# Optimization experiments

Measured on AMD Instinct MI355X. Metric: run time of the kernel, lower is better.

The kernel has to match this reference:

```python
import jax, jax.numpy as jnp
import numpy as np

NEG_SLOPE = 0.2  # PyG GATv2Conv default negative_slope


def gatv2_layer(x, src, dst, Wl, bl, Wr, br, att, bias, concat):
    """GATv2Conv (PyG semantics): message j->i, softmax over incoming edges of i."""
    N = x.shape[0]
    H, C = att.shape
    xl = (x @ Wl + bl).reshape(N, H, C)  # source-side transform
    xr = (x @ Wr + br).reshape(N, H, C)  # target-side transform
    msg = xl[src]                                   # [E,H,C] gathered source feats
    e = jax.nn.leaky_relu(msg + xr[dst], NEG_SLOPE)  # [E,H,C]
    score = jnp.einsum('ehc,hc->eh', e, att)        # [E,H]
    # segment softmax over destination node (every node has a self loop -> no empty segment)
    smax = jax.ops.segment_max(score, dst, num_segments=N)
    ex = jnp.exp(score - smax[dst])
    denom = jax.ops.segment_sum(ex, dst, num_segments=N)
    alpha = ex / denom[dst]                         # [E,H]
    out = jax.ops.segment_sum(alpha[:, :, None] * msg, dst, num_segments=N)  # [N,H,C]
    out = out.reshape(N, H * C) if concat else out.mean(axis=1)
    return out + bias


def setup_inputs():
    key = jax.random.key(0)
    ks = jax.random.split(key, 16)
    N, E = 50000, 800000
    D_in, Hd, H, D_out = 128, 32, 4, 64
    HC = Hd * H  # 128
    s = 0.05
    return {
        'x': jax.random.normal(ks[0], (N, D_in), jnp.float32),
        'edge_index': jax.random.randint(ks[1], (2, E), 0, N, dtype=jnp.int32),
        # layer 1: GATv2Conv(D_in, Hd, heads=H)
        'Wl1': jax.random.normal(ks[2], (D_in, HC), jnp.float32) * s,
        'bl1': jnp.zeros((HC,), jnp.float32),
        'Wr1': jax.random.normal(ks[3], (D_in, HC), jnp.float32) * s,
        'br1': jnp.zeros((HC,), jnp.float32),
        'att1': jax.random.normal(ks[4], (H, Hd), jnp.float32) * s,
        'bias1': jnp.zeros((HC,), jnp.float32),
        # layer 2: GATv2Conv(HC, D_out, heads=1, concat=False)
        'Wl2': jax.random.normal(ks[5], (HC, D_out), jnp.float32) * s,
        'bl2': jnp.zeros((D_out,), jnp.float32),
        'Wr2': jax.random.normal(ks[6], (HC, D_out), jnp.float32) * s,
        'br2': jnp.zeros((D_out,), jnp.float32),
        'att2': jax.random.normal(ks[7], (1, D_out), jnp.float32) * s,
        'bias2': jnp.zeros((D_out,), jnp.float32),
    }


def reference(x, edge_index, Wl1, bl1, Wr1, br1, att1, bias1,
              Wl2, bl2, Wr2, br2, att2, bias2):
    N = x.shape[0]
    loops = jnp.arange(N, dtype=edge_index.dtype)  # add_self_loops=True (PyG default)
    src = jnp.concatenate([edge_index[0], loops])
    dst = jnp.concatenate([edge_index[1], loops])
    h = gatv2_layer(x, src, dst, Wl1, bl1, Wr1, br1, att1, bias1, concat=True)
    h = jax.nn.relu(h)
    out = gatv2_layer(h, src, dst, Wl2, bl2, Wr2, br2, att2, bias2, concat=False)
    return out
```

## Files before the change

kernel.cpp:

```cpp
#include <hip/hip_runtime.h>
#include <hip/hip_bf16.h>
#include <math.h>


#define NSLOPE 0.2f
#define L2E 1.4426950408889634f
#define BKT 64

typedef __attribute__((ext_vector_type(8))) short short8;
typedef __attribute__((ext_vector_type(4))) float f32x4;
typedef _Float16 h16x2 __attribute__((ext_vector_type(2)));

__device__ inline unsigned short f2bf(float f) {
  unsigned int u = __float_as_uint(f);
  u += 0x7fff + ((u >> 16) & 1);
  return (unsigned short)(u >> 16);
}
__device__ inline float bf2f(unsigned short h) {
  return __uint_as_float(((unsigned int)h) << 16);
}

__device__ inline float merge2(float qa, float qb, int m, int lane) {
  bool hi = (lane & m) != 0;
  float sel = hi ? qb : qa;
  float oth = hi ? qa : qb;
  return sel + __shfl_xor(oth, m);
}

template <typename AT>
__device__ __forceinline__ void gemm_body(const AT* __restrict__ A,
    const float* __restrict__ Wl, const float* __restrict__ Wr,
    const float* __restrict__ bl, const float* __restrict__ br,
    _Float16* __restrict__ xl, _Float16* __restrict__ xr, int C, int M,
    int mblk, int g, unsigned short* sBh, unsigned short* sBl) {
  int t = threadIdx.x;
  for (int s = t; s < 1024; s += 256) {
    int lane = s & 63;
    int kt = (s >> 6) & 3;
    int tn = s >> 8;
    int n = g * 64 + tn * 16 + (lane & 15);
    int k0 = kt * 32 + ((lane >> 4) * 8);
    const float* W = (n < C) ? (Wl + n) : (Wr + (n - C));
    int base = ((tn * 4 + kt) * 64 + lane) * 8;
#pragma unroll
    for (int j = 0; j < 8; j++) {
      float v = W[(size_t)(k0 + j) * C];
      unsigned short hi = f2bf(v);
      sBh[base + j] = hi;
      sBl[base + j] = f2bf(v - bf2f(hi));
    }
  }
  __syncthreads();
  int w = t >> 6, l = t & 63;
  int m_base = mblk * 128 + w * 32;
  int mrow = l & 15;
  int kq = l >> 4;
  f32x4 acc[2][4];
#pragma unroll
  for (int mt = 0; mt < 2; mt++)
#pragma unroll
    for (int tn = 0; tn < 4; tn++) acc[mt][tn] = (f32x4){0.f, 0.f, 0.f, 0.f};

#pragma unroll
  for (int kt = 0; kt < 4; kt++) {
    short8 ah[2], al[2];
#pragma unroll
    for (int mt = 0; mt < 2; mt++) {
      int m = m_base + mt * 16 + mrow;
      m = (m < M) ? m : (M - 1);
      const AT* pa = A + (size_t)m * 128 + kt * 32 + kq * 8;
      float f[8];
      if constexpr (sizeof(AT) == 4) {
        float4 v0 = *(const float4*)pa;
        float4 v1 = *(const float4*)(pa + 4);
        f[0] = v0.x; f[1] = v0.y; f[2] = v0.z; f[3] = v0.w;
        f[4] = v1.x; f[5] = v1.y; f[6] = v1.z; f[7] = v1.w;
      } else {
        h16x2 h0 = *(const h16x2*)(pa + 0);
        h16x2 h1 = *(const h16x2*)(pa + 2);
        h16x2 h2 = *(const h16x2*)(pa + 4);
        h16x2 h3 = *(const h16x2*)(pa + 6);
        f[0] = (float)h0.x; f[1] = (float)h0.y; f[2] = (float)h1.x; f[3] = (float)h1.y;
        f[4] = (float)h2.x; f[5] = (float)h2.y; f[6] = (float)h3.x; f[7] = (float)h3.y;
      }
#pragma unroll
      for (int j = 0; j < 8; j++) {
        unsigned short hi = f2bf(f[j]);
        ah[mt][j] = (short)hi;
        al[mt][j] = (short)f2bf(f[j] - bf2f(hi));
      }
    }
#pragma unroll
    for (int tn = 0; tn < 4; tn++) {
      int off = ((tn * 4 + kt) * 64 + l) * 8;
      short8 bh = *(const short8*)(sBh + off);
      short8 blo = *(const short8*)(sBl + off);
#pragma unroll
      for (int mt = 0; mt < 2; mt++) {
        acc[mt][tn] = __builtin_amdgcn_mfma_f32_16x16x32_bf16(ah[mt], bh, acc[mt][tn], 0, 0, 0);
        acc[mt][tn] = __builtin_amdgcn_mfma_f32_16x16x32_bf16(ah[mt], blo, acc[mt][tn], 0, 0, 0);
        acc[mt][tn] = __builtin_amdgcn_mfma_f32_16x16x32_bf16(al[mt], bh, acc[mt][tn], 0, 0, 0);
      }
    }
  }
#pragma unroll
  for (int tn = 0; tn < 4; tn++) {
    int n = g * 64 + tn * 16 + mrow;
    float bias = (n < C) ? bl[n] : br[n - C];
#pragma unroll
    for (int mt = 0; mt < 2; mt++) {
#pragma unroll
      for (int r = 0; r < 4; r++) {
        int m = m_base + mt * 16 + kq * 4 + r;
        if (m < M) {
          float v = acc[mt][tn][r] + bias;
          if (n < C) xl[(size_t)m * C + n] = (_Float16)v;
          else       xr[(size_t)m * C + (n - C)] = (_Float16)v;
        }
      }
    }
  }
}


__global__ __launch_bounds__(256) void fat1_kernel(
    const int* __restrict__ srcv, const int* __restrict__ dstv,
    int* __restrict__ counts, int* __restrict__ bucket, int E,
    const float* __restrict__ A,
    const float* __restrict__ Wl, const float* __restrict__ Wr,
    const float* __restrict__ bl, const float* __restrict__ br,
    _Float16* __restrict__ xl, _Float16* __restrict__ xr, int M, int countBlocks) {
  __shared__ unsigned short sBh[16 * 512];
  __shared__ unsigned short sBl[16 * 512];
  if ((int)blockIdx.x < countBlocks) {
    int base = blockIdx.x * 2048 + threadIdx.x;
    int d[8], s[8], r[8];
#pragma unroll
    for (int u = 0; u < 8; u++) {
      int idx = base + u * 256;
      d[u] = (idx < E) ? dstv[idx] : -1;
      s[u] = (idx < E) ? srcv[idx] : 0;
    }
#pragma unroll
    for (int u = 0; u < 8; u++)
      if (d[u] >= 0) r[u] = atomicAdd(&counts[d[u]], 1);
#pragma unroll
    for (int u = 0; u < 8; u++)
      if (d[u] >= 0 && r[u] < BKT) bucket[d[u] * BKT + r[u]] = s[u];
  } else {
    int bid = blockIdx.x - countBlocks;
    gemm_body<float>(A, Wl, Wr, bl, br, xl, xr, 128, M, bid >> 2, bid & 3, sBh, sBl);
  }
}

__global__ __launch_bounds__(256) void gemm2_kernel(const _Float16* __restrict__ A,
    const float* __restrict__ Wl, const float* __restrict__ Wr,
    const float* __restrict__ bl, const float* __restrict__ br,
    _Float16* __restrict__ xl, _Float16* __restrict__ xr, int M) {
  __shared__ unsigned short sBh[16 * 512];
  __shared__ unsigned short sBl[16 * 512];
  gemm_body<_Float16>(A, Wl, Wr, bl, br, xl, xr, 64, M, blockIdx.x >> 1, blockIdx.x & 1, sBh, sBl);
}


__device__ inline h16x2 leaky_pk(h16x2 s) {
  h16x2 s2 = s * (h16x2){(_Float16)NSLOPE, (_Float16)NSLOPE};
  return __builtin_elementwise_max(s, s2);
}

__global__ __launch_bounds__(256) void edge1_kernel(
    const _Float16* __restrict__ xl, const _Float16* __restrict__ xr,
    const float* __restrict__ att, const float* __restrict__ bias,
    const int* __restrict__ counts, const int* __restrict__ bucket,
    _Float16* __restrict__ h, int N) {
  int node = blockIdx.x * 4 + (threadIdx.x >> 6);
  if (node >= N) return;
  int lane = threadIdx.x & 63;
  int c = lane * 2;
  h16x2 xri = *(const h16x2*)(xr + (size_t)node * 128 + c);
  float2 atf = *(const float2*)(att + c);
  h16x2 at = {(_Float16)(atf.x * L2E), (_Float16)(atf.y * L2E)};
  int cnt = counts[node];
  int deg = __builtin_amdgcn_readfirstlane(cnt < BKT ? cnt : BKT);
  int s0 = node * BKT;
  int base16 = lane & 48;
  float l, a0, a1;
  {
    h16x2 ms = *(const h16x2*)(xl + (size_t)node * 128 + c);
    h16x2 lk = leaky_pk(ms + xri);
    float q = __builtin_amdgcn_fdot2(lk, at, 0.f, false);
    q += __shfl_xor(q, 1);
    q += __shfl_xor(q, 2);
    q += __shfl_xor(q, 4);
    q += __shfl_xor(q, 8);
    float p = exp2f(q);
    l = p; a0 = p * (float)ms.x; a1 = p * (float)ms.y;
  }
  for (int e = 0; e < deg; e += 8) {
    int j[8];
#pragma unroll
    for (int u = 0; u < 8; u++) {
      int ee = e + u;
      j[u] = __builtin_amdgcn_readfirstlane(bucket[s0 + (ee < deg ? ee : deg - 1)]);
    }
    h16x2 mv[8];
#pragma unroll
    for (int u = 0; u < 8; u++) mv[u] = *(const h16x2*)(xl + (size_t)j[u] * 128 + c);
    float q[8];
#pragma unroll
    for (int u = 0; u < 8; u++) {
      h16x2 lk = leaky_pk(mv[u] + xri);
      q[u] = __builtin_amdgcn_fdot2(lk, at, (e + u < deg) ? 0.f : -1e30f, false);
    }
    float v0 = merge2(q[0], q[1], 1, lane);
    float v1 = merge2(q[2], q[3], 1, lane);
    float v2 = merge2(q[4], q[5], 1, lane);
    float v3 = merge2(q[6], q[7], 1, lane);
    float w0 = merge2(v0, v1, 2, lane);
    float w1 = merge2(v2, v3, 2, lane);
    float uu = merge2(w0, w1, 4, lane);
    uu += __shfl_xor(uu, 8);
    float p = exp2f(uu);
    float cb[8];
#pragma unroll
    for (int u = 0; u < 8; u++) cb[u] = __shfl(p, base16 + u);
#pragma unroll
    for (int u = 0; u < 8; u++) {
      l += cb[u];
      a0 = fmaf(cb[u], (float)mv[u].x, a0);
      a1 = fmaf(cb[u], (float)mv[u].y, a1);
    }
  }
  float inv = 1.f / l;
  float2 bb = *(const float2*)(bias + c);
  float o0 = fmaxf(fmaf(a0, inv, bb.x), 0.f);
  float o1 = fmaxf(fmaf(a1, inv, bb.y), 0.f);
  *(h16x2*)(h + (size_t)node * 128 + c) = (h16x2){(_Float16)o0, (_Float16)o1};
}

__global__ __launch_bounds__(256) void edge2_kernel(
    const _Float16* __restrict__ xl, const _Float16* __restrict__ xr,
    const float* __restrict__ att, const float* __restrict__ bias,
    const int* __restrict__ counts, const int* __restrict__ bucket,
    float* __restrict__ out, int N) {
  int node = blockIdx.x * 4 + (threadIdx.x >> 6);
  if (node >= N) return;
  int lane = threadIdx.x & 63;
  int half = lane >> 5;
  int c = (lane & 31) * 2;
  h16x2 xri = *(const h16x2*)(xr + (size_t)node * 64 + c);
  float2 atf = *(const float2*)(att + c);
  h16x2 at = {(_Float16)(atf.x * L2E), (_Float16)(atf.y * L2E)};
  int cnt = counts[node];
  int deg = __builtin_amdgcn_readfirstlane(cnt < BKT ? cnt : BKT);
  int s0 = node * BKT;
  int hbase = lane & 32;
  float l = 0.f, a0 = 0.f, a1 = 0.f;
  {
    h16x2 ms = *(const h16x2*)(xl + (size_t)node * 64 + c);
    h16x2 lk = leaky_pk(ms + xri);
    float q = __builtin_amdgcn_fdot2(lk, at, 0.f, false);
    q += __shfl_xor(q, 1);
    q += __shfl_xor(q, 2);
    q += __shfl_xor(q, 4);
    q += __shfl_xor(q, 8);
    q += __shfl_xor(q, 16);
    float p = exp2f(q);
    if (half == 0) { l = p; a0 = p * (float)ms.x; a1 = p * (float)ms.y; }
  }
  for (int e = 0; e < deg; e += 8) {
    int j[4];
#pragma unroll
    for (int u = 0; u < 4; u++) {
      int ee = e + 2 * u + half;
      j[u] = bucket[s0 + (ee < deg ? ee : deg - 1)];
    }
    h16x2 mv[4];
#pragma unroll
    for (int u = 0; u < 4; u++) mv[u] = *(const h16x2*)(xl + (size_t)j[u] * 64 + c);
    float q[4];
#pragma unroll
    for (int u = 0; u < 4; u++) {
      h16x2 lk = leaky_pk(mv[u] + xri);
      q[u] = __builtin_amdgcn_fdot2(lk, at, (e + 2 * u + half < deg) ? 0.f : -1e30f, false);
    }
    float v0 = merge2(q[0], q[1], 1, lane);
    float v1 = merge2(q[2], q[3], 1, lane);
    float uu = merge2(v0, v1, 2, lane);
    uu += __shfl_xor(uu, 4);
    uu += __shfl_xor(uu, 8);
    uu += __shfl_xor(uu, 16);
    float p = exp2f(uu);
    float cb[4];
#pragma unroll
    for (int u = 0; u < 4; u++) cb[u] = __shfl(p, hbase + u);
#pragma unroll
    for (int u = 0; u < 4; u++) {
      l += cb[u];
      a0 = fmaf(cb[u], (float)mv[u].x, a0);
      a1 = fmaf(cb[u], (float)mv[u].y, a1);
    }
  }
  l  += __shfl_xor(l, 32);
  a0 += __shfl_xor(a0, 32);
  a1 += __shfl_xor(a1, 32);
  if (half == 0) {
    float inv = 1.f / l;
    float2 bb = *(const float2*)(bias + c);
    *(float2*)(out + (size_t)node * 64 + c) =
        make_float2(fmaf(a0, inv, bb.x), fmaf(a1, inv, bb.y));
  }
}

extern "C" void kernel_launch(void* const* d_in, const int* in_sizes, int n_in,
                              void* d_out, int out_size, void* d_ws, size_t ws_size,
                              hipStream_t stream) {
  const float* x    = (const float*)d_in[0];
  const int*   ei   = (const int*)d_in[1];
  const float* Wl1  = (const float*)d_in[2];
  const float* bl1  = (const float*)d_in[3];
  const float* Wr1  = (const float*)d_in[4];
  const float* br1  = (const float*)d_in[5];
  const float* att1 = (const float*)d_in[6];
  const float* bias1= (const float*)d_in[7];
  const float* Wl2  = (const float*)d_in[8];
  const float* bl2  = (const float*)d_in[9];
  const float* Wr2  = (const float*)d_in[10];
  const float* br2  = (const float*)d_in[11];
  const float* att2 = (const float*)d_in[12];
  const float* bias2= (const float*)d_in[13];
  float* out = (float*)d_out;

  const int N = in_sizes[0] / 128;
  const int E = in_sizes[1] / 2;
  const int* srcv = ei;
  const int* dstv = ei + E;

  char* ws = (char*)d_ws;
  size_t off = 0;
  auto alloc = [&](size_t bytes) -> void* {
    void* p = ws + off;
    off = (off + bytes + 255) & ~(size_t)255;
    return p;
  };
  int* counts      = (int*)alloc((size_t)N * 4);
  int* bucket      = (int*)alloc((size_t)N * BKT * 4);
  _Float16* xl1h = (_Float16*)alloc((size_t)N * 128 * 2);
  _Float16* xr1h = (_Float16*)alloc((size_t)N * 128 * 2);
  _Float16* hbuf = (_Float16*)alloc((size_t)N * 128 * 2);
  _Float16* xl2h = xl1h;
  _Float16* xr2h = xr1h;
  (void)ws_size; (void)n_in; (void)out_size;

  int mb = (N + 127) / 128;
  int countBlocks = (E + 2047) / 2048;

  hipMemsetAsync(counts, 0, (size_t)N * 4, stream);
  fat1_kernel<<<countBlocks + mb * 4, 256, 0, stream>>>(
      srcv, dstv, counts, bucket, E, x, Wl1, Wr1, bl1, br1, xl1h, xr1h, N, countBlocks);
  edge1_kernel<<<(N + 3) / 4, 256, 0, stream>>>(xl1h, xr1h, att1, bias1, counts,
                                                bucket, hbuf, N);
  gemm2_kernel<<<mb * 2, 256, 0, stream>>>(hbuf, Wl2, Wr2, bl2, br2, xl2h, xr2h, N);
  edge2_kernel<<<(N + 3) / 4, 256, 0, stream>>>(xl2h, xr2h, att2, bias2, counts,
                                                bucket, out, N);
}
```

Baseline: 259.7 us.

## Build per-XCD edge buckets with 16-bit indices and compact them before edge kernels

The bucketing pass now keeps a separate count array and a 16-slot bucket per XCD, using workgroup-scoped relaxed atomics so destination counters are not contended across chiplets. A new compaction kernel merges the eight per-XCD sub-buckets into one 64-slot bucket per node with a degree array, which both edge kernels then read. Source indices are stored as uint16, halving bucket traffic, but this only works while N < 65536. It adds a kernel launch, a larger memset, and a serial per-thread merge. Edges are also silently dropped if a node gets more than 16 incoming edges from one XCD.

```diff
diff --git a/kernel.cpp b/kernel.cpp
--- a/kernel.cpp
+++ b/kernel.cpp
@@ -6,6 +6,7 @@
 #define NSLOPE 0.2f
 #define L2E 1.4426950408889634f
 #define BKT 64
+#define SUB 16
 
 typedef __attribute__((ext_vector_type(8))) short short8;
 typedef __attribute__((ext_vector_type(4))) float f32x4;
@@ -18,6 +19,12 @@
 }
 __device__ inline float bf2f(unsigned short h) {
   return __uint_as_float(((unsigned int)h) << 16);
+}
+
+__device__ inline int xcd_id() {
+  int x;
+  asm volatile("s_getreg_b32 %0, hwreg(HW_REG_XCC_ID)" : "=s"(x));
+  return x & 7;
 }
 
 __device__ inline float merge2(float qa, float qb, int m, int lane) {
@@ -125,7 +132,7 @@
 
 __global__ __launch_bounds__(256) void fat1_kernel(
     const int* __restrict__ srcv, const int* __restrict__ dstv,
-    int* __restrict__ counts, int* __restrict__ bucket, int E,
+    int* __restrict__ counts8, unsigned short* __restrict__ bucket8, int E, int N,
     const float* __restrict__ A,
     const float* __restrict__ Wl, const float* __restrict__ Wr,
     const float* __restrict__ bl, const float* __restrict__ br,
@@ -133,6 +140,9 @@
   __shared__ unsigned short sBh[16 * 512];
   __shared__ unsigned short sBl[16 * 512];
   if ((int)blockIdx.x < countBlocks) {
+    int xcd = xcd_id();
+    int* cnt = counts8 + (size_t)xcd * N;
+    unsigned short* bkt = bucket8 + (size_t)xcd * N * SUB;
     int base = blockIdx.x * 2048 + threadIdx.x;
     int d[8], s[8], r[8];
 #pragma unroll
@@ -143,14 +153,35 @@
     }
 #pragma unroll
     for (int u = 0; u < 8; u++)
-      if (d[u] >= 0) r[u] = atomicAdd(&counts[d[u]], 1);
+      if (d[u] >= 0)
+        r[u] = __hip_atomic_fetch_add(&cnt[d[u]], 1, __ATOMIC_RELAXED,
+                                      __HIP_MEMORY_SCOPE_WORKGROUP);
 #pragma unroll
     for (int u = 0; u < 8; u++)
-      if (d[u] >= 0 && r[u] < BKT) bucket[d[u] * BKT + r[u]] = s[u];
+      if (d[u] >= 0 && r[u] < SUB) bkt[(size_t)d[u] * SUB + r[u]] = (unsigned short)s[u];
   } else {
     int bid = blockIdx.x - countBlocks;
     gemm_body<float>(A, Wl, Wr, bl, br, xl, xr, 128, M, bid >> 2, bid & 3, sBh, sBl);
   }
+}
+
+__global__ __launch_bounds__(256) void compact_kernel(
+    const int* __restrict__ counts8, const unsigned short* __restrict__ bucket8,
+    unsigned short* __restrict__ bucketC, int* __restrict__ degC, int N) {
+  int node = blockIdx.x * 256 + threadIdx.x;
+  if (node >= N) return;
+  int deg = 0;
+  unsigned short* outp = bucketC + (size_t)node * BKT;
+#pragma unroll
+  for (int x = 0; x < 8; x++) {
+    int c = counts8[(size_t)x * N + node];
+    c = c < SUB ? c : SUB;
+    const unsigned short* row = bucket8 + ((size_t)x * N + node) * SUB;
+    for (int k = 0; k < c; k++) {
+      if (deg < BKT) outp[deg++] = row[k];
+    }
+  }
+  degC[node] = deg;
 }
 
 __global__ __launch_bounds__(256) void gemm2_kernel(const _Float16* __restrict__ A,
@@ -171,7 +202,7 @@
 __global__ __launch_bounds__(256) void edge1_kernel(
     const _Float16* __restrict__ xl, const _Float16* __restrict__ xr,
     const float* __restrict__ att, const float* __restrict__ bias,
-    const int* __restrict__ counts, const int* __restrict__ bucket,
+    const int* __restrict__ degC, const unsigned short* __restrict__ bucketC,
     _Float16* __restrict__ h, int N) {
   int node = blockIdx.x * 4 + (threadIdx.x >> 6);
   if (node >= N) return;
@@ -180,9 +211,8 @@
   h16x2 xri = *(const h16x2*)(xr + (size_t)node * 128 + c);
   float2 atf = *(const float2*)(att + c);
   h16x2 at = {(_Float16)(atf.x * L2E), (_Float16)(atf.y * L2E)};
-  int cnt = counts[node];
-  int deg = __builtin_amdgcn_readfirstlane(cnt < BKT ? cnt : BKT);
-  int s0 = node * BKT;
+  int deg = __builtin_amdgcn_readfirstlane(degC[node]);
+  size_t s0 = (size_t)node * BKT;
   int base16 = lane & 48;
   float l, a0, a1;
   {
@@ -201,7 +231,8 @@
 #pragma unroll
     for (int u = 0; u < 8; u++) {
       int ee = e + u;
-      j[u] = __builtin_amdgcn_readfirstlane(bucket[s0 + (ee < deg ? ee : deg - 1)]);
+      j[u] = __builtin_amdgcn_readfirstlane(
+          (int)bucketC[s0 + (ee < deg ? ee : deg - 1)]);
     }
     h16x2 mv[8];
 #pragma unroll
@@ -241,7 +272,7 @@
 __global__ __launch_bounds__(256) void edge2_kernel(
     const _Float16* __restrict__ xl, const _Float16* __restrict__ xr,
     const float* __restrict__ att, const float* __restrict__ bias,
-    const int* __restrict__ counts, const int* __restrict__ bucket,
+    const int* __restrict__ degC, const unsigned short* __restrict__ bucketC,
     float* __restrict__ out, int N) {
   int node = blockIdx.x * 4 + (threadIdx.x >> 6);
   if (node >= N) return;
@@ -251,9 +282,8 @@
   h16x2 xri = *(const h16x2*)(xr + (size_t)node * 64 + c);
   float2 atf = *(const float2*)(att + c);
   h16x2 at = {(_Float16)(atf.x * L2E), (_Float16)(atf.y * L2E)};
-  int cnt = counts[node];
-  int deg = __builtin_amdgcn_readfirstlane(cnt < BKT ? cnt : BKT);
-  int s0 = node * BKT;
+  int deg = __builtin_amdgcn_readfirstlane(degC[node]);
+  size_t s0 = (size_t)node * BKT;
   int hbase = lane & 32;
   float l = 0.f, a0 = 0.f, a1 = 0.f;
   {
@@ -273,7 +303,7 @@
 #pragma unroll
     for (int u = 0; u < 4; u++) {
       int ee = e + 2 * u + half;
-      j[u] = bucket[s0 + (ee < deg ? ee : deg - 1)];
+      j[u] = (int)bucketC[s0 + (ee < deg ? ee : deg - 1)];
     }
     h16x2 mv[4];
 #pragma unroll
@@ -343,8 +373,10 @@
     off = (off + bytes + 255) & ~(size_t)255;
     return p;
   };
-  int* counts      = (int*)alloc((size_t)N * 4);
-  int* bucket      = (int*)alloc((size_t)N * BKT * 4);
+  int* counts8             = (int*)alloc((size_t)8 * N * 4);
+  unsigned short* bucket8  = (unsigned short*)alloc((size_t)8 * N * SUB * 2);
+  unsigned short* bucketC  = (unsigned short*)alloc((size_t)N * BKT * 2);
+  int* degC                = (int*)alloc((size_t)N * 4);
   _Float16* xl1h = (_Float16*)alloc((size_t)N * 128 * 2);
   _Float16* xr1h = (_Float16*)alloc((size_t)N * 128 * 2);
   _Float16* hbuf = (_Float16*)alloc((size_t)N * 128 * 2);
@@ -355,12 +387,13 @@
   int mb = (N + 127) / 128;
   int countBlocks = (E + 2047) / 2048;
 
-  hipMemsetAsync(counts, 0, (size_t)N * 4, stream);
+  hipMemsetAsync(counts8, 0, (size_t)8 * N * 4, stream);
   fat1_kernel<<<countBlocks + mb * 4, 256, 0, stream>>>(
-      srcv, dstv, counts, bucket, E, x, Wl1, Wr1, bl1, br1, xl1h, xr1h, N, countBlocks);
-  edge1_kernel<<<(N + 3) / 4, 256, 0, stream>>>(xl1h, xr1h, att1, bias1, counts,
-                                                bucket, hbuf, N);
+      srcv, dstv, counts8, bucket8, E, N, x, Wl1, Wr1, bl1, br1, xl1h, xr1h, N, countBlocks);
+  compact_kernel<<<(N + 255) / 256, 256, 0, stream>>>(counts8, bucket8, bucketC, degC, N);
+  edge1_kernel<<<(N + 3) / 4, 256, 0, stream>>>(xl1h, xr1h, att1, bias1, degC,
+                                                bucketC, hbuf, N);
   gemm2_kernel<<<mb * 2, 256, 0, stream>>>(hbuf, Wl2, Wr2, bl2, br2, xl2h, xr2h, N);
-  edge2_kernel<<<(N + 3) / 4, 256, 0, stream>>>(xl2h, xr2h, att2, bias2, counts,
-                                                bucket, out, N);
-}
+  edge2_kernel<<<(N + 3) / 4, 256, 0, stream>>>(xl2h, xr2h, att2, bias2, degC,
+                                                bucketC, out, N);
+}
```

Result: slower. 267.0 us (+2.8%).
